# Kernel tuning notes

Measured on AMD Instinct MI355X. Metric: run time of the kernel, lower is better.

## Reference

```python
import jax, jax.numpy as jnp
import numpy as np

# Irrep structure (fixed by init_kwargs):
#   irreps_in      = 128x0e + 128x1o          -> x: [N, 128 + 128*3] = [N, 512]
#   irreps_nonlin  = 32x0e + 16x1o            (16 scalars + 16 gates + 16 gated vectors)
#   hidden_irreps  = 16x0e + 16x1o            (Gate output)
#   irreps_out     = 10x0e + 1x1o             -> out: [N, 13]
MUL_IN = 128
N_SCAL = 16   # gated-block scalars
N_GATE = 16   # gate scalars
N_VEC = 16    # gated 1o multiplicity
NUM_ELEM = 10


def setup_inputs() -> dict:
    key = jax.random.key(0)
    ks = jax.random.split(key, 8)
    N = 100000
    x = jax.random.normal(ks[0], (N, MUL_IN * 4), dtype=jnp.float32)  # 128 scalars + 128 vectors
    # o3.Linear weights: N(0,1) init, one (mul_in, mul_out) block per matching irrep pair
    W1_s = jax.random.normal(ks[1], (MUL_IN, N_SCAL + N_GATE), dtype=jnp.float32)  # 128x0e -> 32x0e
    W1_v = jax.random.normal(ks[2], (MUL_IN, N_VEC), dtype=jnp.float32)            # 128x1o -> 16x1o
    b1_s = jax.random.normal(ks[3], (N_SCAL + N_GATE,), dtype=jnp.float32) * 0.1   # bias on 0e only
    W2_s = jax.random.normal(ks[4], (N_SCAL, NUM_ELEM), dtype=jnp.float32)         # 16x0e -> 10x0e
    W2_v = jax.random.normal(ks[5], (N_VEC, 1), dtype=jnp.float32)                 # 16x1o -> 1x1o
    b2_s = jax.random.normal(ks[6], (NUM_ELEM,), dtype=jnp.float32) * 0.1
    return {"x": x, "W1_s": W1_s, "W1_v": W1_v, "b1_s": b1_s,
            "W2_s": W2_s, "W2_v": W2_v, "b2_s": b2_s}


def reference(x, W1_s, W1_v, b1_s, W2_s, W2_v, b2_s):
    N = x.shape[0]
    inv1 = 1.0 / np.sqrt(MUL_IN)   # o3.Linear path normalization (single path per output)
    inv2s = 1.0 / np.sqrt(N_SCAL)
    inv2v = 1.0 / np.sqrt(N_VEC)

    x_s = x[:, :MUL_IN]                               # [N, 128] scalars (0e)
    x_v = x[:, MUL_IN:].reshape(N, MUL_IN, 3)         # [N, 128, 3] vectors (1o)

    # linear_1: irreps_in -> irreps_nonlin (bias on scalar outputs only)
    h_s = x_s @ W1_s * inv1 + b1_s                    # [N, 32]
    h_v = jnp.einsum('nic,io->noc', x_v, W1_v) * inv1 # [N, 16, 3]

    # Gate: silu on scalars; silu(gates) elementwise-scales gated vectors
    scalars = jax.nn.silu(h_s[:, :N_SCAL])            # [N, 16]
    gates = jax.nn.silu(h_s[:, N_SCAL:])              # [N, 16]
    gated_v = gates[:, :, None] * h_v                 # [N, 16, 3]

    # linear_2: hidden_irreps -> irreps_out (10x0e + 1x1o)
    out_s = scalars @ W2_s * inv2s + b2_s             # [N, 10]
    out_v = jnp.einsum('nic,io->noc', gated_v, W2_v) * inv2v  # [N, 1, 3]
    return jnp.concatenate([out_s, out_v.reshape(N, 3)], axis=-1)  # [N, 13]
```

## Files before the change

### kernel.cpp

```cpp
#include <hip/hip_runtime.h>
#include <math.h>


typedef short  bf16x8 __attribute__((ext_vector_type(8)));
typedef float  f32x4  __attribute__((ext_vector_type(4)));

static __device__ __forceinline__ short f2bf(float f) {
    union { float f; unsigned u; } v; v.f = f;
    return (short)((v.u + 0x8000u) >> 16);
}

#define BLOCK 256

__global__ __launch_bounds__(BLOCK, 2) void nlrb_kernel(
    const float* __restrict__ x,
    const float* __restrict__ W1s,
    const float* __restrict__ W1v,
    const float* __restrict__ b1s,
    const float* __restrict__ W2s,
    const float* __restrict__ W2v,
    const float* __restrict__ b2s,
    float* __restrict__ out,
    int N)
{
    __shared__ float sred[4][16][68];

    const int tid  = threadIdx.x;
    const int wave = tid >> 6;
    const int lane = tid & 63;
    const int mq   = lane >> 4;
    const int o    = lane & 15;
    const float inv1 = 0.08838834764831843f;

    bf16x8 bS0[4], bS1[4], bV[4];
    #pragma unroll
    for (int kb = 0; kb < 4; ++kb) {
        #pragma unroll
        for (int j = 0; j < 8; ++j) {
            const int k = kb * 32 + mq * 8 + j;
            bS0[kb][j] = f2bf(W1s[k * 32 + o]);
            bS1[kb][j] = f2bf(W1s[k * 32 + 16 + o]);
            bV [kb][j] = f2bf(W1v[k * 16 + o]);
        }
    }
    const int e = o;
    float wcr[16];
    #pragma unroll
    for (int j = 0; j < 16; ++j)
        wcr[j] = (e < 10) ? W2s[j * 10 + e] : W2v[j];
    const float b2e = (e < 10) ? b2s[e] : 0.0f;
    const float b1a = b1s[o];
    const float b1b = b1s[16 + o];

    const int NT = N >> 4;
    const int wstride = gridDim.x << 2;

    for (int wt = (blockIdx.x << 2) + wave; wt < NT; wt += wstride) {
        const int base = wt << 4;
        const float* xp = x + (size_t)(base + o) * 512;

        float4 LS[4][2], LV[4][6];
        #pragma unroll
        for (int kb = 0; kb < 4; ++kb) {
            LS[kb][0] = *(const float4*)(xp + kb * 32 + mq * 8);
            LS[kb][1] = *(const float4*)(xp + kb * 32 + mq * 8 + 4);
        }
        #pragma unroll
        for (int kb = 0; kb < 4; ++kb) {
            #pragma unroll
            for (int q = 0; q < 6; ++q)
                LV[kb][q] = *(const float4*)(xp + 128 + kb * 96 + mq * 24 + q * 4);
        }

        f32x4 accS0 = {0.f,0.f,0.f,0.f}, accS1 = {0.f,0.f,0.f,0.f};
        f32x4 accV0 = {0.f,0.f,0.f,0.f}, accV1 = {0.f,0.f,0.f,0.f};
        f32x4 accV2 = {0.f,0.f,0.f,0.f};

        #pragma unroll
        for (int kb = 0; kb < 4; ++kb) {
            float u[8];
            u[0]=LS[kb][0].x; u[1]=LS[kb][0].y; u[2]=LS[kb][0].z; u[3]=LS[kb][0].w;
            u[4]=LS[kb][1].x; u[5]=LS[kb][1].y; u[6]=LS[kb][1].z; u[7]=LS[kb][1].w;
            bf16x8 a;
            #pragma unroll
            for (int j = 0; j < 8; ++j) a[j] = f2bf(u[j]);
            accS0 = __builtin_amdgcn_mfma_f32_16x16x32_bf16(a, bS0[kb], accS0, 0, 0, 0);
            accS1 = __builtin_amdgcn_mfma_f32_16x16x32_bf16(a, bS1[kb], accS1, 0, 0, 0);
        }
        #pragma unroll
        for (int kb = 0; kb < 4; ++kb) {
            float t[24];
            #pragma unroll
            for (int q = 0; q < 6; ++q) {
                t[4*q+0] = LV[kb][q].x; t[4*q+1] = LV[kb][q].y;
                t[4*q+2] = LV[kb][q].z; t[4*q+3] = LV[kb][q].w;
            }
            bf16x8 a0, a1, a2;
            #pragma unroll
            for (int j = 0; j < 8; ++j) {
                a0[j] = f2bf(t[3*j+0]);
                a1[j] = f2bf(t[3*j+1]);
                a2[j] = f2bf(t[3*j+2]);
            }
            accV0 = __builtin_amdgcn_mfma_f32_16x16x32_bf16(a0, bV[kb], accV0, 0, 0, 0);
            accV1 = __builtin_amdgcn_mfma_f32_16x16x32_bf16(a1, bV[kb], accV1, 0, 0, 0);
            accV2 = __builtin_amdgcn_mfma_f32_16x16x32_bf16(a2, bV[kb], accV2, 0, 0, 0);
        }

        #pragma unroll
        for (int v = 0; v < 4; ++v) {
            const float hs = fmaf(accS0[v], inv1, b1a);
            const float hg = fmaf(accS1[v], inv1, b1b);
            const float s  = hs / (1.f + __expf(-hs));
            const float g  = hg / (1.f + __expf(-hg));
            const float gm = g * inv1;
            const int  r   = mq * 4 + v;
            sred[wave][r][o]      = s;
            sred[wave][r][16 + o] = gm * accV0[v];
            sred[wave][r][32 + o] = gm * accV1[v];
            sred[wave][r][48 + o] = gm * accV2[v];
        }
        asm volatile("s_waitcnt lgkmcnt(0)" ::: "memory");

        #pragma unroll
        for (int w = 0; w < 4; ++w) {
            const int r = (w << 2) + mq;
            if (e < 13) {
                const int slot = (e < 10) ? 0 : (e - 9);
                const float* p = &sred[wave][r][slot * 16];
                float sum = 0.f;
                #pragma unroll
                for (int j = 0; j < 16; ++j)
                    sum = fmaf(p[j], wcr[j], sum);
                out[(size_t)(base + r) * 13 + e] = fmaf(sum, 0.25f, b2e);
            }
        }
        asm volatile("s_waitcnt lgkmcnt(0)" ::: "memory");
    }
}

extern "C" void kernel_launch(void* const* d_in, const int* in_sizes, int n_in,
                              void* d_out, int out_size, void* d_ws, size_t ws_size,
                              hipStream_t stream) {
    const float* x   = (const float*)d_in[0];
    const float* W1s = (const float*)d_in[1];
    const float* W1v = (const float*)d_in[2];
    const float* b1s = (const float*)d_in[3];
    const float* W2s = (const float*)d_in[4];
    const float* W2v = (const float*)d_in[5];
    const float* b2s = (const float*)d_in[6];
    float* outp = (float*)d_out;
    const int N = in_sizes[0] / 512;
    nlrb_kernel<<<dim3(512), dim3(BLOCK), 0, stream>>>(
        x, W1s, W1v, b1s, W2s, W2v, b2s, outp, N);
}
```

Baseline: 41.80 us.

## Stage x through swizzled LDS as bf16 with coalesced loads and register prefetch

Each wave now loads its 16-row tile with fully coalesced float4 loads, converts it to bf16, and stores it into a per-wave swizzled LDS buffer. The MFMA operands are then read from LDS as packed bf16x8. The next tile is prefetched into registers while the current one is computed. This replaces strided per-row global loads with coalesced ones and overlaps HBM latency with compute, at the cost of 64 KB of LDS per block and 128 extra prefetch registers, which may reduce occupancy.

```diff
diff --git a/kernel.cpp b/kernel.cpp
--- a/kernel.cpp
+++ b/kernel.cpp
@@ -3,6 +3,7 @@
 
 
 typedef short  bf16x8 __attribute__((ext_vector_type(8)));
+typedef short  short4v __attribute__((ext_vector_type(4)));
 typedef float  f32x4  __attribute__((ext_vector_type(4)));
 
 static __device__ __forceinline__ short f2bf(float f) {
@@ -23,7 +24,7 @@
     float* __restrict__ out,
     int N)
 {
-    __shared__ float sred[4][16][68];
+    __shared__ __align__(16) char smem[4][16384];
 
     const int tid  = threadIdx.x;
     const int wave = tid >> 6;
@@ -31,6 +32,7 @@
     const int mq   = lane >> 4;
     const int o    = lane & 15;
     const float inv1 = 0.08838834764831843f;
+    char* const wbase = smem[wave];
 
     bf16x8 bS0[4], bS1[4], bV[4];
     #pragma unroll
@@ -54,59 +56,76 @@
 
     const int NT = N >> 4;
     const int wstride = gridDim.x << 2;
+    const int wt0 = (blockIdx.x << 2) + wave;
+    const int sw = (o & 7) << 4;
 
-    for (int wt = (blockIdx.x << 2) + wave; wt < NT; wt += wstride) {
+    float4 L[32];
+    if (wt0 < NT) {
+        const float4* src = (const float4*)(x + (size_t)(wt0 << 4) * 512);
+        #pragma unroll
+        for (int s = 0; s < 32; ++s)
+            L[s] = src[s * 64 + lane];
+    }
+
+    for (int wt = wt0; wt < NT; wt += wstride) {
         const int base = wt << 4;
-        const float* xp = x + (size_t)(base + o) * 512;
 
-        float4 LS[4][2], LV[4][6];
         #pragma unroll
-        for (int kb = 0; kb < 4; ++kb) {
-            LS[kb][0] = *(const float4*)(xp + kb * 32 + mq * 8);
-            LS[kb][1] = *(const float4*)(xp + kb * 32 + mq * 8 + 4);
-        }
-        #pragma unroll
-        for (int kb = 0; kb < 4; ++kb) {
-            #pragma unroll
-            for (int q = 0; q < 6; ++q)
-                LV[kb][q] = *(const float4*)(xp + 128 + kb * 96 + mq * 24 + q * 4);
+        for (int s = 0; s < 32; ++s) {
+            const int F = s * 256 + lane * 4;
+            const int r = F >> 9;
+            const int byte = r * 1024 + (((F & 511) * 2) ^ ((r & 7) << 4));
+            short4v h;
+            h[0] = f2bf(L[s].x); h[1] = f2bf(L[s].y);
+            h[2] = f2bf(L[s].z); h[3] = f2bf(L[s].w);
+            *(short4v*)(wbase + byte) = h;
         }
 
+        const int nxt = wt + wstride;
+        if (nxt < NT) {
+            const float4* src = (const float4*)(x + (size_t)(nxt << 4) * 512);
+            #pragma unroll
+            for (int s = 0; s < 32; ++s)
+                L[s] = src[s * 64 + lane];
+        }
+
+        asm volatile("s_waitcnt lgkmcnt(0)" ::: "memory");
+
+        const char* rb = wbase + o * 1024;
         f32x4 accS0 = {0.f,0.f,0.f,0.f}, accS1 = {0.f,0.f,0.f,0.f};
         f32x4 accV0 = {0.f,0.f,0.f,0.f}, accV1 = {0.f,0.f,0.f,0.f};
         f32x4 accV2 = {0.f,0.f,0.f,0.f};
 
         #pragma unroll
         for (int kb = 0; kb < 4; ++kb) {
-            float u[8];
-            u[0]=LS[kb][0].x; u[1]=LS[kb][0].y; u[2]=LS[kb][0].z; u[3]=LS[kb][0].w;
-            u[4]=LS[kb][1].x; u[5]=LS[kb][1].y; u[6]=LS[kb][1].z; u[7]=LS[kb][1].w;
-            bf16x8 a;
-            #pragma unroll
-            for (int j = 0; j < 8; ++j) a[j] = f2bf(u[j]);
+            bf16x8 a = *(const bf16x8*)(rb + ((kb * 64 + mq * 16) ^ sw));
             accS0 = __builtin_amdgcn_mfma_f32_16x16x32_bf16(a, bS0[kb], accS0, 0, 0, 0);
             accS1 = __builtin_amdgcn_mfma_f32_16x16x32_bf16(a, bS1[kb], accS1, 0, 0, 0);
         }
         #pragma unroll
         for (int kb = 0; kb < 4; ++kb) {
-            float t[24];
+            short t[24];
             #pragma unroll
-            for (int q = 0; q < 6; ++q) {
-                t[4*q+0] = LV[kb][q].x; t[4*q+1] = LV[kb][q].y;
-                t[4*q+2] = LV[kb][q].z; t[4*q+3] = LV[kb][q].w;
+            for (int q = 0; q < 3; ++q) {
+                bf16x8 tq = *(const bf16x8*)(
+                    rb + ((256 + kb * 192 + mq * 48 + q * 16) ^ sw));
+                #pragma unroll
+                for (int i = 0; i < 8; ++i) t[q * 8 + i] = tq[i];
             }
             bf16x8 a0, a1, a2;
             #pragma unroll
             for (int j = 0; j < 8; ++j) {
-                a0[j] = f2bf(t[3*j+0]);
-                a1[j] = f2bf(t[3*j+1]);
-                a2[j] = f2bf(t[3*j+2]);
+                a0[j] = t[3 * j + 0];
+                a1[j] = t[3 * j + 1];
+                a2[j] = t[3 * j + 2];
             }
             accV0 = __builtin_amdgcn_mfma_f32_16x16x32_bf16(a0, bV[kb], accV0, 0, 0, 0);
             accV1 = __builtin_amdgcn_mfma_f32_16x16x32_bf16(a1, bV[kb], accV1, 0, 0, 0);
             accV2 = __builtin_amdgcn_mfma_f32_16x16x32_bf16(a2, bV[kb], accV2, 0, 0, 0);
         }
 
+        asm volatile("s_waitcnt lgkmcnt(0)" ::: "memory");
+        float* const sredw = (float*)wbase;
         #pragma unroll
         for (int v = 0; v < 4; ++v) {
             const float hs = fmaf(accS0[v], inv1, b1a);
@@ -115,10 +134,10 @@
             const float g  = hg / (1.f + __expf(-hg));
             const float gm = g * inv1;
             const int  r   = mq * 4 + v;
-            sred[wave][r][o]      = s;
-            sred[wave][r][16 + o] = gm * accV0[v];
-            sred[wave][r][32 + o] = gm * accV1[v];
-            sred[wave][r][48 + o] = gm * accV2[v];
+            sredw[r * 68 + o]      = s;
+            sredw[r * 68 + 16 + o] = gm * accV0[v];
+            sredw[r * 68 + 32 + o] = gm * accV1[v];
+            sredw[r * 68 + 48 + o] = gm * accV2[v];
         }
         asm volatile("s_waitcnt lgkmcnt(0)" ::: "memory");
 
@@ -127,11 +146,16 @@
             const int r = (w << 2) + mq;
             if (e < 13) {
                 const int slot = (e < 10) ? 0 : (e - 9);
-                const float* p = &sred[wave][r][slot * 16];
+                const float4* p = (const float4*)(sredw + r * 68 + slot * 16);
                 float sum = 0.f;
                 #pragma unroll
-                for (int j = 0; j < 16; ++j)
-                    sum = fmaf(p[j], wcr[j], sum);
+                for (int q = 0; q < 4; ++q) {
+                    float4 pv = p[q];
+                    sum = fmaf(pv.x, wcr[q * 4 + 0], sum);
+                    sum = fmaf(pv.y, wcr[q * 4 + 1], sum);
+                    sum = fmaf(pv.z, wcr[q * 4 + 2], sum);
+                    sum = fmaf(pv.w, wcr[q * 4 + 3], sum);
+                }
                 out[(size_t)(base + r) * 13 + e] = fmaf(sum, 0.25f, b2e);
             }
         }
```

New measurement: 53.41 us. 1.28x slower.

## Software-pipeline x loads across tiles and use packed bf16 conversion

Applied to the files above, without the earlier changes.

Input rows for the next wave tile are prefetched into registers while the current tile's MFMAs run, so global memory latency overlaps with compute. The scalar f2bf conversions become v_cvt_pk_bf16_f32 plus byte-permutes that de-interleave the xyz vector components, and the LDS reduction reads float4 instead of scalars. The double-buffered register set raises register pressure, which may limit occupancy. The packed convert may round differently from the old add-and-shift version.

```diff
diff --git a/kernel.cpp b/kernel.cpp
--- a/kernel.cpp
+++ b/kernel.cpp
@@ -3,11 +3,17 @@
 
 
 typedef short  bf16x8 __attribute__((ext_vector_type(8)));
+typedef int    i32x4  __attribute__((ext_vector_type(4)));
 typedef float  f32x4  __attribute__((ext_vector_type(4)));
 
 static __device__ __forceinline__ short f2bf(float f) {
     union { float f; unsigned u; } v; v.f = f;
     return (short)((v.u + 0x8000u) >> 16);
+}
+static __device__ __forceinline__ unsigned cvtpk(float lo, float hi) {
+    unsigned r;
+    asm("v_cvt_pk_bf16_f32 %0, %1, %2" : "=v"(r) : "v"(lo), "v"(hi));
+    return r;
 }
 
 #define BLOCK 256
@@ -54,23 +60,26 @@
 
     const int NT = N >> 4;
     const int wstride = gridDim.x << 2;
+    const int wt0 = (blockIdx.x << 2) + wave;
 
-    for (int wt = (blockIdx.x << 2) + wave; wt < NT; wt += wstride) {
-        const int base = wt << 4;
-        const float* xp = x + (size_t)(base + o) * 512;
-
-        float4 LS[4][2], LV[4][6];
+    float4 LS[4][2], LV[4][6];
+    if (wt0 < NT) {
+        const float* xp = x + (size_t)((wt0 << 4) + o) * 512;
         #pragma unroll
         for (int kb = 0; kb < 4; ++kb) {
             LS[kb][0] = *(const float4*)(xp + kb * 32 + mq * 8);
             LS[kb][1] = *(const float4*)(xp + kb * 32 + mq * 8 + 4);
-        }
-        #pragma unroll
-        for (int kb = 0; kb < 4; ++kb) {
             #pragma unroll
             for (int q = 0; q < 6; ++q)
                 LV[kb][q] = *(const float4*)(xp + 128 + kb * 96 + mq * 24 + q * 4);
         }
+    }
+
+    for (int wt = wt0; wt < NT; wt += wstride) {
+        const int base = wt << 4;
+        const int nxt  = wt + wstride;
+        const int nb   = (nxt < NT) ? nxt : wt;
+        const float* xq = x + (size_t)((nb << 4) + o) * 512;
 
         f32x4 accS0 = {0.f,0.f,0.f,0.f}, accS1 = {0.f,0.f,0.f,0.f};
         f32x4 accV0 = {0.f,0.f,0.f,0.f}, accV1 = {0.f,0.f,0.f,0.f};
@@ -78,30 +87,39 @@
 
         #pragma unroll
         for (int kb = 0; kb < 4; ++kb) {
-            float u[8];
-            u[0]=LS[kb][0].x; u[1]=LS[kb][0].y; u[2]=LS[kb][0].z; u[3]=LS[kb][0].w;
-            u[4]=LS[kb][1].x; u[5]=LS[kb][1].y; u[6]=LS[kb][1].z; u[7]=LS[kb][1].w;
-            bf16x8 a;
-            #pragma unroll
-            for (int j = 0; j < 8; ++j) a[j] = f2bf(u[j]);
+            i32x4 wv;
+            wv[0] = (int)cvtpk(LS[kb][0].x, LS[kb][0].y);
+            wv[1] = (int)cvtpk(LS[kb][0].z, LS[kb][0].w);
+            wv[2] = (int)cvtpk(LS[kb][1].x, LS[kb][1].y);
+            wv[3] = (int)cvtpk(LS[kb][1].z, LS[kb][1].w);
+            LS[kb][0] = *(const float4*)(xq + kb * 32 + mq * 8);
+            LS[kb][1] = *(const float4*)(xq + kb * 32 + mq * 8 + 4);
+            const bf16x8 a = __builtin_bit_cast(bf16x8, wv);
             accS0 = __builtin_amdgcn_mfma_f32_16x16x32_bf16(a, bS0[kb], accS0, 0, 0, 0);
             accS1 = __builtin_amdgcn_mfma_f32_16x16x32_bf16(a, bS1[kb], accS1, 0, 0, 0);
         }
+
         #pragma unroll
         for (int kb = 0; kb < 4; ++kb) {
-            float t[24];
+            unsigned p[12];
             #pragma unroll
             for (int q = 0; q < 6; ++q) {
-                t[4*q+0] = LV[kb][q].x; t[4*q+1] = LV[kb][q].y;
-                t[4*q+2] = LV[kb][q].z; t[4*q+3] = LV[kb][q].w;
+                p[2*q]   = cvtpk(LV[kb][q].x, LV[kb][q].y);
+                p[2*q+1] = cvtpk(LV[kb][q].z, LV[kb][q].w);
             }
-            bf16x8 a0, a1, a2;
             #pragma unroll
-            for (int j = 0; j < 8; ++j) {
-                a0[j] = f2bf(t[3*j+0]);
-                a1[j] = f2bf(t[3*j+1]);
-                a2[j] = f2bf(t[3*j+2]);
+            for (int q = 0; q < 6; ++q)
+                LV[kb][q] = *(const float4*)(xq + 128 + kb * 96 + mq * 24 + q * 4);
+            i32x4 w0, w1, w2;
+            #pragma unroll
+            for (int w = 0; w < 4; ++w) {
+                w0[w] = (int)__builtin_amdgcn_perm(p[3*w+1], p[3*w],   0x07060100u);
+                w1[w] = (int)__builtin_amdgcn_perm(p[3*w+2], p[3*w],   0x05040302u);
+                w2[w] = (int)__builtin_amdgcn_perm(p[3*w+2], p[3*w+1], 0x07060100u);
             }
+            const bf16x8 a0 = __builtin_bit_cast(bf16x8, w0);
+            const bf16x8 a1 = __builtin_bit_cast(bf16x8, w1);
+            const bf16x8 a2 = __builtin_bit_cast(bf16x8, w2);
             accV0 = __builtin_amdgcn_mfma_f32_16x16x32_bf16(a0, bV[kb], accV0, 0, 0, 0);
             accV1 = __builtin_amdgcn_mfma_f32_16x16x32_bf16(a1, bV[kb], accV1, 0, 0, 0);
             accV2 = __builtin_amdgcn_mfma_f32_16x16x32_bf16(a2, bV[kb], accV2, 0, 0, 0);
@@ -127,11 +145,16 @@
             const int r = (w << 2) + mq;
             if (e < 13) {
                 const int slot = (e < 10) ? 0 : (e - 9);
-                const float* p = &sred[wave][r][slot * 16];
+                const float4* pp = (const float4*)(&sred[wave][r][slot * 16]);
                 float sum = 0.f;
                 #pragma unroll
-                for (int j = 0; j < 16; ++j)
-                    sum = fmaf(p[j], wcr[j], sum);
+                for (int q = 0; q < 4; ++q) {
+                    float4 pv = pp[q];
+                    sum = fmaf(pv.x, wcr[q * 4 + 0], sum);
+                    sum = fmaf(pv.y, wcr[q * 4 + 1], sum);
+                    sum = fmaf(pv.z, wcr[q * 4 + 2], sum);
+                    sum = fmaf(pv.w, wcr[q * 4 + 3], sum);
+                }
                 out[(size_t)(base + r) * 13 + e] = fmaf(sum, 0.25f, b2e);
             }
         }
```

Measured after the change: 47.96 us. +14.7%, slower.

## Software-pipeline x loads across tiles, move weights to LDS, double occupancy

Applied to the files above, without the earlier changes.

Restructures the per-wave loop into a two-buffer software pipeline. The global loads for the next k-block, and for the first two k-blocks of the next tile, are issued while the current block is converted and fed to MFMA. The B-operand weights and the second-layer weights move from registers into shared memory, which frees VGPRs. Launch bounds go to 4 blocks per CU and the grid doubles. Conversion to bf16 now uses packed v_cvt_pk_bf16_f32 plus byte permutes instead of scalar rounding; this rounding may differ slightly from the old manual round-half-up, and the extra LDS reads could add latency.

```diff
diff --git a/kernel.cpp b/kernel.cpp
--- a/kernel.cpp
+++ b/kernel.cpp
@@ -2,17 +2,23 @@
 #include <math.h>
 
 
-typedef short  bf16x8 __attribute__((ext_vector_type(8)));
-typedef float  f32x4  __attribute__((ext_vector_type(4)));
+typedef short bf16x8 __attribute__((ext_vector_type(8)));
+typedef int   i32x4  __attribute__((ext_vector_type(4)));
+typedef float f32x4  __attribute__((ext_vector_type(4)));
 
 static __device__ __forceinline__ short f2bf(float f) {
     union { float f; unsigned u; } v; v.f = f;
     return (short)((v.u + 0x8000u) >> 16);
 }
+static __device__ __forceinline__ unsigned cvtpk(float lo, float hi) {
+    unsigned r;
+    asm("v_cvt_pk_bf16_f32 %0, %1, %2" : "=v"(r) : "v"(lo), "v"(hi));
+    return r;
+}
 
 #define BLOCK 256
 
-__global__ __launch_bounds__(BLOCK, 2) void nlrb_kernel(
+__global__ __launch_bounds__(BLOCK, 4) void nlrb_kernel(
     const float* __restrict__ x,
     const float* __restrict__ W1s,
     const float* __restrict__ W1v,
@@ -23,7 +29,11 @@
     float* __restrict__ out,
     int N)
 {
-    __shared__ float sred[4][16][68];
+    __shared__ bf16x8 BS0[4][4][16];
+    __shared__ bf16x8 BS1[4][4][16];
+    __shared__ bf16x8 BVv[4][4][16];
+    __shared__ float  WC[16][20];
+    __shared__ float  sred[4][16][68];
 
     const int tid  = threadIdx.x;
     const int wave = tid >> 6;
@@ -32,80 +42,111 @@
     const int o    = lane & 15;
     const float inv1 = 0.08838834764831843f;
 
-    bf16x8 bS0[4], bS1[4], bV[4];
-    #pragma unroll
-    for (int kb = 0; kb < 4; ++kb) {
+    {
+        const int kb = tid >> 6, m = (tid >> 4) & 3, oo = tid & 15;
+        bf16x8 t0, t1, t2;
         #pragma unroll
         for (int j = 0; j < 8; ++j) {
-            const int k = kb * 32 + mq * 8 + j;
-            bS0[kb][j] = f2bf(W1s[k * 32 + o]);
-            bS1[kb][j] = f2bf(W1s[k * 32 + 16 + o]);
-            bV [kb][j] = f2bf(W1v[k * 16 + o]);
+            const int k = kb * 32 + m * 8 + j;
+            t0[j] = f2bf(W1s[k * 32 + oo]);
+            t1[j] = f2bf(W1s[k * 32 + 16 + oo]);
+            t2[j] = f2bf(W1v[k * 16 + oo]);
+        }
+        BS0[kb][m][oo] = t0;
+        BS1[kb][m][oo] = t1;
+        BVv[kb][m][oo] = t2;
+        if (tid < 16) {
+            #pragma unroll
+            for (int j = 0; j < 16; ++j)
+                WC[tid][j] = (tid < 10) ? W2s[j * 10 + tid] : W2v[j];
         }
     }
-    const int e = o;
-    float wcr[16];
-    #pragma unroll
-    for (int j = 0; j < 16; ++j)
-        wcr[j] = (e < 10) ? W2s[j * 10 + e] : W2v[j];
-    const float b2e = (e < 10) ? b2s[e] : 0.0f;
+    __syncthreads();
+
     const float b1a = b1s[o];
     const float b1b = b1s[16 + o];
+    const float b2e = (o < 10) ? b2s[o] : 0.0f;
 
     const int NT = N >> 4;
     const int wstride = gridDim.x << 2;
-
-    for (int wt = (blockIdx.x << 2) + wave; wt < NT; wt += wstride) {
+    const int wt0 = (blockIdx.x << 2) + wave;
+    const size_t pfoff = (size_t)wstride * 8192;
+
+#define ISSUE(A, xp, kb)                                                     \
+    do {                                                                     \
+        A[0] = *(const float4*)((xp) + (kb) * 32 + mq * 8);                  \
+        A[1] = *(const float4*)((xp) + (kb) * 32 + mq * 8 + 4);              \
+        _Pragma("unroll")                                                    \
+        for (int q = 0; q < 6; ++q)                                          \
+            A[2 + q] = *(const float4*)((xp) + 128 + (kb) * 96 + mq * 24 + q * 4); \
+    } while (0)
+
+#define CONV(A, aS, a0, a1, a2)                                              \
+    do {                                                                     \
+        i32x4 ws;                                                            \
+        ws[0] = (int)cvtpk(A[0].x, A[0].y); ws[1] = (int)cvtpk(A[0].z, A[0].w); \
+        ws[2] = (int)cvtpk(A[1].x, A[1].y); ws[3] = (int)cvtpk(A[1].z, A[1].w); \
+        aS = __builtin_bit_cast(bf16x8, ws);                                 \
+        unsigned p[12];                                                      \
+        _Pragma("unroll")                                                    \
+        for (int q = 0; q < 6; ++q) {                                        \
+            p[2 * q]     = cvtpk(A[2 + q].x, A[2 + q].y);                    \
+            p[2 * q + 1] = cvtpk(A[2 + q].z, A[2 + q].w);                    \
+        }                                                                    \
+        i32x4 w0, w1, w2;                                                    \
+        _Pragma("unroll")                                                    \
+        for (int w = 0; w < 4; ++w) {                                        \
+            w0[w] = (int)__builtin_amdgcn_perm(p[3*w+1], p[3*w],   0x07060100u); \
+            w1[w] = (int)__builtin_amdgcn_perm(p[3*w+2], p[3*w],   0x05040302u); \
+            w2[w] = (int)__builtin_amdgcn_perm(p[3*w+2], p[3*w+1], 0x07060100u); \
+        }                                                                    \
+        a0 = __builtin_bit_cast(bf16x8, w0);                                 \
+        a1 = __builtin_bit_cast(bf16x8, w1);                                 \
+        a2 = __builtin_bit_cast(bf16x8, w2);                                 \
+    } while (0)
+
+#define MF(kb, aS, a0, a1, a2)                                               \
+    do {                                                                     \
+        const bf16x8 q0 = BS0[kb][mq][o];                                    \
+        const bf16x8 q1 = BS1[kb][mq][o];                                    \
+        const bf16x8 q2 = BVv[kb][mq][o];                                    \
+        accS0 = __builtin_amdgcn_mfma_f32_16x16x32_bf16(aS, q0, accS0, 0, 0, 0); \
+        accS1 = __builtin_amdgcn_mfma_f32_16x16x32_bf16(aS, q1, accS1, 0, 0, 0); \
+        accV0 = __builtin_amdgcn_mfma_f32_16x16x32_bf16(a0, q2, accV0, 0, 0, 0); \
+        accV1 = __builtin_amdgcn_mfma_f32_16x16x32_bf16(a1, q2, accV1, 0, 0, 0); \
+        accV2 = __builtin_amdgcn_mfma_f32_16x16x32_bf16(a2, q2, accV2, 0, 0, 0); \
+    } while (0)
+
+    float4 A0[8], A1[8];
+    if (wt0 < NT) {
+        const float* xp = x + (size_t)((wt0 << 4) + o) * 512;
+        ISSUE(A0, xp, 0);
+        ISSUE(A1, xp, 1);
+    }
+
+    for (int wt = wt0; wt < NT; wt += wstride) {
         const int base = wt << 4;
         const float* xp = x + (size_t)(base + o) * 512;
-
-        float4 LS[4][2], LV[4][6];
-        #pragma unroll
-        for (int kb = 0; kb < 4; ++kb) {
-            LS[kb][0] = *(const float4*)(xp + kb * 32 + mq * 8);
-            LS[kb][1] = *(const float4*)(xp + kb * 32 + mq * 8 + 4);
-        }
-        #pragma unroll
-        for (int kb = 0; kb < 4; ++kb) {
-            #pragma unroll
-            for (int q = 0; q < 6; ++q)
-                LV[kb][q] = *(const float4*)(xp + 128 + kb * 96 + mq * 24 + q * 4);
-        }
+        const bool pf = (wt + wstride) < NT;
+        const float* xq = xp + pfoff;
 
         f32x4 accS0 = {0.f,0.f,0.f,0.f}, accS1 = {0.f,0.f,0.f,0.f};
         f32x4 accV0 = {0.f,0.f,0.f,0.f}, accV1 = {0.f,0.f,0.f,0.f};
         f32x4 accV2 = {0.f,0.f,0.f,0.f};
-
-        #pragma unroll
-        for (int kb = 0; kb < 4; ++kb) {
-            float u[8];
-            u[0]=LS[kb][0].x; u[1]=LS[kb][0].y; u[2]=LS[kb][0].z; u[3]=LS[kb][0].w;
-            u[4]=LS[kb][1].x; u[5]=LS[kb][1].y; u[6]=LS[kb][1].z; u[7]=LS[kb][1].w;
-            bf16x8 a;
-            #pragma unroll
-            for (int j = 0; j < 8; ++j) a[j] = f2bf(u[j]);
-            accS0 = __builtin_amdgcn_mfma_f32_16x16x32_bf16(a, bS0[kb], accS0, 0, 0, 0);
-            accS1 = __builtin_amdgcn_mfma_f32_16x16x32_bf16(a, bS1[kb], accS1, 0, 0, 0);
-        }
-        #pragma unroll
-        for (int kb = 0; kb < 4; ++kb) {
-            float t[24];
-            #pragma unroll
-            for (int q = 0; q < 6; ++q) {
-                t[4*q+0] = LV[kb][q].x; t[4*q+1] = LV[kb][q].y;
-                t[4*q+2] = LV[kb][q].z; t[4*q+3] = LV[kb][q].w;
-            }
-            bf16x8 a0, a1, a2;
-            #pragma unroll
-            for (int j = 0; j < 8; ++j) {
-                a0[j] = f2bf(t[3*j+0]);
-                a1[j] = f2bf(t[3*j+1]);
-                a2[j] = f2bf(t[3*j+2]);
-            }
-            accV0 = __builtin_amdgcn_mfma_f32_16x16x32_bf16(a0, bV[kb], accV0, 0, 0, 0);
-            accV1 = __builtin_amdgcn_mfma_f32_16x16x32_bf16(a1, bV[kb], accV1, 0, 0, 0);
-            accV2 = __builtin_amdgcn_mfma_f32_16x16x32_bf16(a2, bV[kb], accV2, 0, 0, 0);
-        }
+        bf16x8 aS, a0, a1, a2;
+
+        CONV(A0, aS, a0, a1, a2);
+        ISSUE(A0, xp, 2);
+        MF(0, aS, a0, a1, a2);
+        CONV(A1, aS, a0, a1, a2);
+        ISSUE(A1, xp, 3);
+        MF(1, aS, a0, a1, a2);
+        CONV(A0, aS, a0, a1, a2);
+        if (pf) ISSUE(A0, xq, 0);
+        MF(2, aS, a0, a1, a2);
+        CONV(A1, aS, a0, a1, a2);
+        if (pf) ISSUE(A1, xq, 1);
+        MF(3, aS, a0, a1, a2);
 
         #pragma unroll
         for (int v = 0; v < 4; ++v) {
@@ -125,18 +166,27 @@
         #pragma unroll
         for (int w = 0; w < 4; ++w) {
             const int r = (w << 2) + mq;
-            if (e < 13) {
-                const int slot = (e < 10) ? 0 : (e - 9);
-                const float* p = &sred[wave][r][slot * 16];
+            if (o < 13) {
+                const int slot = (o < 10) ? 0 : (o - 9);
+                const float* sp = &sred[wave][r][slot * 16];
                 float sum = 0.f;
                 #pragma unroll
-                for (int j = 0; j < 16; ++j)
-                    sum = fmaf(p[j], wcr[j], sum);
-                out[(size_t)(base + r) * 13 + e] = fmaf(sum, 0.25f, b2e);
+                for (int q = 0; q < 4; ++q) {
+                    const float4 pv = *(const float4*)(sp + q * 4);
+                    const float4 wv = *(const float4*)(&WC[o][q * 4]);
+                    sum = fmaf(pv.x, wv.x, sum);
+                    sum = fmaf(pv.y, wv.y, sum);
+                    sum = fmaf(pv.z, wv.z, sum);
+                    sum = fmaf(pv.w, wv.w, sum);
+                }
+                out[(size_t)(base + r) * 13 + o] = fmaf(sum, 0.25f, b2e);
             }
         }
         asm volatile("s_waitcnt lgkmcnt(0)" ::: "memory");
     }
+#undef ISSUE
+#undef CONV
+#undef MF
 }
 
 extern "C" void kernel_launch(void* const* d_in, const int* in_sizes, int n_in,
@@ -151,6 +201,6 @@
     const float* b2s = (const float*)d_in[6];
     float* outp = (float*)d_out;
     const int N = in_sizes[0] / 512;
-    nlrb_kernel<<<dim3(512), dim3(BLOCK), 0, stream>>>(
+    nlrb_kernel<<<dim3(1024), dim3(BLOCK), 0, stream>>>(
         x, W1s, W1v, b1s, W2s, W2v, b2s, outp, N);
 }
```

New measurement: 52.30 us. 25.1% more time.
